# Kernel optimization log

Measured on AMD Instinct MI355X. Metric: run time of the kernel, lower is better.

The kernel has to match this reference:

```python
import jax, jax.numpy as jnp
import numpy as np

Q = 4          # base of nested scalar quantizer (config.q)
M = 2          # hierarchy depth (config.M)
LEVELS = Q ** M  # total number of representable integer levels
SCALE = 60.0   # manual scale_factor passed to the layer
EPS = 1e-8


def _scalar_quantize(x):
    # Symmetric nested-lattice scalar quantizer over q^M integer levels:
    # round to nearest integer, clip to the symmetric range covered by the
    # M-level base-q codebook.
    half = LEVELS // 2
    return jnp.clip(jnp.round(x), -half, half - 1)


def _ste_quantize_weight(w):
    # Per-row L2 norm scaling -> unit-norm rows -> scale by SCALE -> quantize
    # -> rescale back (matches ScalarStraightThroughQuantize.forward).
    row_norms = jnp.linalg.norm(w, axis=1, keepdims=True)          # [out, 1]
    row_norms_safe = jnp.maximum(row_norms, EPS)
    w_scaled = w / row_norms_safe * SCALE
    q = _scalar_quantize(w_scaled)
    return q * row_norms_safe / SCALE


def setup_inputs() -> dict:
    key = jax.random.key(0)
    k1, k2 = jax.random.split(key)
    BATCH, IN_F, OUT_F = 8192, 4096, 4096
    x = jax.random.normal(k1, (BATCH, IN_F), dtype=jnp.float32)
    # weight initialized as randn * 0.1 per the module
    weight = jax.random.normal(k2, (OUT_F, IN_F), dtype=jnp.float32) * 0.1
    bias = jnp.zeros((OUT_F,), dtype=jnp.float32)
    return {"x": x, "weight": weight, "bias": bias}


def reference(x, weight, bias):
    # STE: forward uses the quantized weight; gradient is identity through
    # the quantizer (stop_gradient trick).
    w_q = weight + jax.lax.stop_gradient(_ste_quantize_weight(weight) - weight)
    return x @ w_q.T + bias
```

## Files before the change

### kernel.cpp

```cpp
#include <hip/hip_runtime.h>
#include <hip/hip_bf16.h>


typedef int int32x4 __attribute__((ext_vector_type(4)));

#define MDIM 8192
#define NDIM 4096
#define KDIM 4096

__device__ __forceinline__ void async_copy16(const void* g, void* l) {
  __builtin_amdgcn_global_load_lds(
      (const __attribute__((address_space(1))) void*)g,
      (__attribute__((address_space(3))) void*)l, 16, 0, 0);
}

__device__ __forceinline__ unsigned pack4(float a, float b, float c, float d) {
  return ((unsigned)((int)a & 0xff)) | ((unsigned)((int)b & 0xff) << 8) |
         ((unsigned)((int)c & 0xff) << 16) | ((unsigned)((int)d & 0xff) << 24);
}

__global__ __launch_bounds__(256) void quantize_all(
    const float* __restrict__ w, const float* __restrict__ x,
    unsigned* __restrict__ qw, unsigned* __restrict__ qx,
    float* __restrict__ scale, float* __restrict__ sx) {
  const int t = threadIdx.x;
  __shared__ float wred[4];
  if (blockIdx.x < NDIM) {
    const int row = blockIdx.x;
    const float4* wr = (const float4*)(w + (size_t)row * KDIM);
    float4 v[4];
    float ss = 0.f;
#pragma unroll
    for (int i = 0; i < 4; ++i) {
      v[i] = wr[t + 256 * i];
      ss += v[i].x * v[i].x + v[i].y * v[i].y + v[i].z * v[i].z + v[i].w * v[i].w;
    }
#pragma unroll
    for (int m = 32; m >= 1; m >>= 1) ss += __shfl_xor(ss, m, 64);
    if ((t & 63) == 0) wred[t >> 6] = ss;
    __syncthreads();
    const float safe = fmaxf(sqrtf(wred[0] + wred[1] + wred[2] + wred[3]), 1e-8f);
    unsigned* qr = qw + (size_t)row * (KDIM / 4);
#pragma unroll
    for (int i = 0; i < 4; ++i) {
      float q0 = fminf(fmaxf(rintf(v[i].x / safe * 60.0f), -8.f), 7.f);
      float q1 = fminf(fmaxf(rintf(v[i].y / safe * 60.0f), -8.f), 7.f);
      float q2 = fminf(fmaxf(rintf(v[i].z / safe * 60.0f), -8.f), 7.f);
      float q3 = fminf(fmaxf(rintf(v[i].w / safe * 60.0f), -8.f), 7.f);
      qr[t + 256 * i] = pack4(q0, q1, q2, q3);
    }
    if (t == 0) scale[row] = safe / 60.0f;
  } else {
    const int row = blockIdx.x - NDIM;
    const float4* xr = (const float4*)(x + (size_t)row * KDIM);
    float4 v[4];
    float am = 0.f;
#pragma unroll
    for (int i = 0; i < 4; ++i) {
      v[i] = xr[t + 256 * i];
      am = fmaxf(am, fmaxf(fmaxf(fabsf(v[i].x), fabsf(v[i].y)),
                           fmaxf(fabsf(v[i].z), fabsf(v[i].w))));
    }
#pragma unroll
    for (int m = 32; m >= 1; m >>= 1) am = fmaxf(am, __shfl_xor(am, m, 64));
    if ((t & 63) == 0) wred[t >> 6] = am;
    __syncthreads();
    const float amax =
        fmaxf(fmaxf(fmaxf(wred[0], wred[1]), fmaxf(wred[2], wred[3])), 1e-20f);
    const float r = 127.0f / amax;
    unsigned* qr = qx + (size_t)row * (KDIM / 4);
#pragma unroll
    for (int i = 0; i < 4; ++i) {
      float q0 = fminf(fmaxf(rintf(v[i].x * r), -127.f), 127.f);
      float q1 = fminf(fmaxf(rintf(v[i].y * r), -127.f), 127.f);
      float q2 = fminf(fmaxf(rintf(v[i].z * r), -127.f), 127.f);
      float q3 = fminf(fmaxf(rintf(v[i].w * r), -127.f), 127.f);
      qr[t + 256 * i] = pack4(q0, q1, q2, q3);
    }
    if (t == 0) sx[row] = amax / 127.0f;
  }
}

__global__ __launch_bounds__(256) void gemm_i8(const char* __restrict__ A,
                                               const char* __restrict__ B,
                                               const float* __restrict__ sx,
                                               const float* __restrict__ scale,
                                               const float* __restrict__ bias,
                                               float* __restrict__ C) {
  __shared__ __align__(16) char sA[128 * 128];
  __shared__ __align__(16) char sB[128 * 128];
  const int tid = threadIdx.x;
  const int m0 = blockIdx.y * 128;
  const int n0 = blockIdx.x * 128;

  const int r0 = tid >> 3;
  const int c16 = ((tid & 7) ^ ((tid >> 3) & 7)) * 16;
  const char* gA = A + (size_t)(m0 + r0) * KDIM + c16;
  const char* gB = B + (size_t)(n0 + r0) * KDIM + c16;
  char* lA = sA + tid * 16;
  char* lB = sB + tid * 16;

  const int lane = tid & 63;
  const int wid = tid >> 6;
  const int wm = (wid & 1) * 64;
  const int wn = (wid >> 1) * 64;
  const int fr = lane & 15;
  const int q = lane >> 4;
  const int sw = fr & 7;
  const int ph0 = ((q) ^ sw) * 16;
  const int ph1 = ((4 + q) ^ sw) * 16;

  int32x4 acc[4][4] = {};

  for (int kt = 0; kt < KDIM / 128; ++kt) {
    __syncthreads();
#pragma unroll
    for (int i = 0; i < 4; ++i) {
      async_copy16(gA + (size_t)(32 * i) * KDIM, lA + i * 4096);
      async_copy16(gB + (size_t)(32 * i) * KDIM, lB + i * 4096);
    }
    __syncthreads();
    gA += 128; gB += 128;

#pragma unroll
    for (int h = 0; h < 2; ++h) {
      const int ph = h ? ph1 : ph0;
      int32x4 af[4], bg[4];
#pragma unroll
      for (int i = 0; i < 4; ++i)
        af[i] = *(const int32x4*)&sA[(wm + i * 16 + fr) * 128 + ph];
#pragma unroll
      for (int j = 0; j < 4; ++j)
        bg[j] = *(const int32x4*)&sB[(wn + j * 16 + fr) * 128 + ph];
#pragma unroll
      for (int i = 0; i < 4; ++i)
#pragma unroll
        for (int j = 0; j < 4; ++j)
          acc[i][j] =
              __builtin_amdgcn_mfma_i32_16x16x64_i8(af[i], bg[j], acc[i][j], 0, 0, 0);
    }
  }

  float scl[4], bs[4];
#pragma unroll
  for (int j = 0; j < 4; ++j) {
    const int n = n0 + wn + j * 16 + fr;
    scl[j] = scale[n];
    bs[j] = bias[n];
  }
  const int mrow = q * 4;
#pragma unroll
  for (int i = 0; i < 4; ++i) {
#pragma unroll
    for (int r = 0; r < 4; ++r) {
      const size_t m = (size_t)(m0 + wm + i * 16 + mrow + r);
      const float sxm = sx[m];
      float* crow = C + m * NDIM + (n0 + wn + fr);
#pragma unroll
      for (int j = 0; j < 4; ++j)
        crow[j * 16] = (float)acc[i][j][r] * (sxm * scl[j]) + bs[j];
    }
  }
}

extern "C" void kernel_launch(void* const* d_in, const int* in_sizes, int n_in,
                              void* d_out, int out_size, void* d_ws, size_t ws_size,
                              hipStream_t stream) {
  (void)in_sizes; (void)n_in; (void)out_size; (void)ws_size;
  const float* x = (const float*)d_in[0];
  const float* w = (const float*)d_in[1];
  const float* bias = (const float*)d_in[2];
  float* out = (float*)d_out;

  char* ws = (char*)d_ws;
  char* qx = ws;
  char* qw = ws + (size_t)33554432;
  float* sx = (float*)(ws + (size_t)50331648);
  float* scale = (float*)(ws + (size_t)50331648 + 65536);

  quantize_all<<<NDIM + MDIM, 256, 0, stream>>>(w, x, (unsigned*)qw,
                                                (unsigned*)qx, scale, sx);
  dim3 grid(NDIM / 128, MDIM / 128);
  gemm_i8<<<grid, 256, 0, stream>>>(qx, qw, sx, scale, bias, out);
}
```

Baseline: 395.9 us.

## Double-buffer LDS tiles in int8 GEMM to overlap loads with MFMA

Result: no change. 402.8 us (+1.7%).

```diff
diff --git a/kernel.cpp b/kernel.cpp
--- a/kernel.cpp
+++ b/kernel.cpp
@@ -87,8 +87,8 @@
                                                const float* __restrict__ scale,
                                                const float* __restrict__ bias,
                                                float* __restrict__ C) {
-  __shared__ __align__(16) char sA[128 * 128];
-  __shared__ __align__(16) char sB[128 * 128];
+  __shared__ __align__(16) char sA[2][128 * 128];
+  __shared__ __align__(16) char sB[2][128 * 128];
   const int tid = threadIdx.x;
   const int m0 = blockIdx.y * 128;
   const int n0 = blockIdx.x * 128;
@@ -97,8 +97,6 @@
   const int c16 = ((tid & 7) ^ ((tid >> 3) & 7)) * 16;
   const char* gA = A + (size_t)(m0 + r0) * KDIM + c16;
   const char* gB = B + (size_t)(n0 + r0) * KDIM + c16;
-  char* lA = sA + tid * 16;
-  char* lB = sB + tid * 16;
 
   const int lane = tid & 63;
   const int wid = tid >> 6;
@@ -112,34 +110,45 @@
 
   int32x4 acc[4][4] = {};
 
-  for (int kt = 0; kt < KDIM / 128; ++kt) {
+#define ISSUE(p)                                                      \
+  do {                                                                \
+    _Pragma("unroll") for (int i = 0; i < 4; ++i) {                   \
+      async_copy16(gA + (size_t)(32 * i) * KDIM,                      \
+                   &sA[p][i * 4096] + tid * 16);                      \
+      async_copy16(gB + (size_t)(32 * i) * KDIM,                      \
+                   &sB[p][i * 4096] + tid * 16);                      \
+    }                                                                 \
+    gA += 128;                                                        \
+    gB += 128;                                                        \
+  } while (0)
+
+#define COMPUTE(p)                                                    \
+  do {                                                                \
+    _Pragma("unroll") for (int h = 0; h < 2; ++h) {                   \
+      const int ph = h ? ph1 : ph0;                                   \
+      int32x4 af[4], bg[4];                                           \
+      _Pragma("unroll") for (int i = 0; i < 4; ++i)                   \
+          af[i] = *(const int32x4*)&sA[p][(wm + i * 16 + fr) * 128 + ph]; \
+      _Pragma("unroll") for (int j = 0; j < 4; ++j)                   \
+          bg[j] = *(const int32x4*)&sB[p][(wn + j * 16 + fr) * 128 + ph]; \
+      _Pragma("unroll") for (int i = 0; i < 4; ++i)                   \
+          _Pragma("unroll") for (int j = 0; j < 4; ++j)               \
+              acc[i][j] = __builtin_amdgcn_mfma_i32_16x16x64_i8(      \
+                  af[i], bg[j], acc[i][j], 0, 0, 0);                  \
+    }                                                                 \
+  } while (0)
+
+  ISSUE(0);
+  for (int kt = 0; kt < KDIM / 128; kt += 2) {
     __syncthreads();
-#pragma unroll
-    for (int i = 0; i < 4; ++i) {
-      async_copy16(gA + (size_t)(32 * i) * KDIM, lA + i * 4096);
-      async_copy16(gB + (size_t)(32 * i) * KDIM, lB + i * 4096);
-    }
+    ISSUE(1);
+    COMPUTE(0);
     __syncthreads();
-    gA += 128; gB += 128;
-
-#pragma unroll
-    for (int h = 0; h < 2; ++h) {
-      const int ph = h ? ph1 : ph0;
-      int32x4 af[4], bg[4];
-#pragma unroll
-      for (int i = 0; i < 4; ++i)
-        af[i] = *(const int32x4*)&sA[(wm + i * 16 + fr) * 128 + ph];
-#pragma unroll
-      for (int j = 0; j < 4; ++j)
-        bg[j] = *(const int32x4*)&sB[(wn + j * 16 + fr) * 128 + ph];
-#pragma unroll
-      for (int i = 0; i < 4; ++i)
-#pragma unroll
-        for (int j = 0; j < 4; ++j)
-          acc[i][j] =
-              __builtin_amdgcn_mfma_i32_16x16x64_i8(af[i], bg[j], acc[i][j], 0, 0, 0);
-    }
+    if (kt + 2 < KDIM / 128) ISSUE(0);
+    COMPUTE(1);
   }
+#undef ISSUE
+#undef COMPUTE
 
   float scl[4], bs[4];
 #pragma unroll
```
